# Performance work log

Hardware: AMD Instinct MI355X
Metric: run time of the kernel (lower is better)

## Reference

```python
import jax, jax.numpy as jnp
import numpy as np

B, H, C, G = 65536, 1024, 2, 2


def setup_inputs() -> dict:
    key = jax.random.key(0)
    ks = jax.random.split(key, 9)
    s = 1.0 / np.sqrt(H)
    return {
        "X": jax.random.normal(ks[0], (B, H), jnp.float32),
        "W_phi": jax.random.normal(ks[1], (H, H), jnp.float32) * s,
        "b_phi": jax.random.normal(ks[2], (H,), jnp.float32) * s,
        "W_groups": jax.random.normal(ks[3], (G, C, H), jnp.float32) * s,
        "b_groups": jax.random.normal(ks[4], (G, C), jnp.float32) * s,
        "W_joint": jax.random.normal(ks[5], (C, H), jnp.float32) * s,
        "b_joint": jax.random.normal(ks[6], (C,), jnp.float32) * s,
        "D": jax.random.randint(ks[7], (B,), 0, G, jnp.int32),
        "D_agn": jax.random.randint(ks[8], (B,), 0, G, jnp.int32),  # models random.random() < ratio
    }


def reference(X, W_phi, b_phi, W_groups, b_groups, W_joint, b_joint, D, D_agn):
    # phi feature extractor: Linear(H -> H)
    phi = X @ W_phi.T + b_phi  # [B, H]
    # Compute both experts' outputs (G=2 is tiny), then gather per-sample.
    all_preds = jnp.einsum("bh,gch->bgc", phi, W_groups) + b_groups[None]  # [B, G, C]
    group_specific = jnp.take_along_axis(all_preds, D[:, None, None].astype(jnp.int32), axis=1)[:, 0]  # [B, C]
    group_agnostic = jnp.take_along_axis(all_preds, D_agn[:, None, None].astype(jnp.int32), axis=1)[:, 0]  # [B, C]
    joint = phi @ W_joint.T + b_joint  # [B, C]
    return (joint, group_specific, group_agnostic)
```

## Files before the change

kernel.cpp:

```cpp
#include <hip/hip_runtime.h>

#define HDIM 1024
#define NR 6

__global__ __launch_bounds__(256) void precompute_kernel(
    const float* __restrict__ Wphi, const float* __restrict__ bphi,
    const float* __restrict__ Wg,  const float* __restrict__ bg,
    const float* __restrict__ Wj,  const float* __restrict__ bj,
    float* __restrict__ A, float* __restrict__ biasEff)
{
    __shared__ float red[256][NR];
    const int t = threadIdx.x;

    if (blockIdx.x == 64) {
        __shared__ float rb[256];
        for (int r = 0; r < NR; ++r) {
            const float* w2 = (r < 2) ? (Wj + r * HDIM) : (Wg + (r - 2) * HDIM);
            float s = 0.f;
            for (int h = t; h < HDIM; h += 256) s += w2[h] * bphi[h];
            rb[t] = s; __syncthreads();
            for (int off = 128; off > 0; off >>= 1) {
                if (t < off) rb[t] += rb[t + off];
                __syncthreads();
            }
            if (t == 0) {
                float b2 = (r < 2) ? bj[r] : bg[r - 2];
                biasEff[r] = rb[0] + b2;
            }
            __syncthreads();
        }
        return;
    }

    const int cb  = blockIdx.x;
    const int col = cb * 16 + (t & 15);
    const int ks  = t >> 4;

    float acc[NR];
    #pragma unroll
    for (int r = 0; r < NR; ++r) acc[r] = 0.f;

    const int h0 = ks * 64;
    #pragma unroll 4
    for (int i = 0; i < 64; ++i) {
        const int h = h0 + i;
        const float w = Wphi[(size_t)h * HDIM + col];
        acc[0] += Wj[h]            * w;
        acc[1] += Wj[HDIM + h]     * w;
        acc[2] += Wg[h]            * w;
        acc[3] += Wg[HDIM + h]     * w;
        acc[4] += Wg[2 * HDIM + h] * w;
        acc[5] += Wg[3 * HDIM + h] * w;
    }
    #pragma unroll
    for (int r = 0; r < NR; ++r) red[t][r] = acc[r];
    __syncthreads();

    if (t < 16 * NR) {
        const int c = t & 15;
        const int r = t >> 4;
        float s = 0.f;
        #pragma unroll
        for (int k = 0; k < 16; ++k) s += red[k * 16 + c][r];
        A[r * HDIM + cb * 16 + c] = s;
    }
}

__global__ __launch_bounds__(256, 3) void main_kernel(
    const float* __restrict__ X, const int* __restrict__ D,
    const int* __restrict__ Dagn,
    const float* __restrict__ A, const float* __restrict__ biasEff,
    float* __restrict__ out, int B)
{
    const int lane  = threadIdx.x & 63;
    const int wave  = threadIdx.x >> 6;
    const int gwave = blockIdx.x * 4 + wave;
    const int nwav  = gridDim.x * 4;

    float4 a[NR][4];
    #pragma unroll
    for (int r = 0; r < NR; ++r) {
        const float4* Ar = (const float4*)(A + r * HDIM);
        #pragma unroll
        for (int j = 0; j < 4; ++j) a[r][j] = Ar[lane + 64 * j];
    }
    float be[NR];
    #pragma unroll
    for (int r = 0; r < NR; ++r) be[r] = biasEff[r];

    for (int b = gwave; b < B; b += nwav) {
        const float4* xr = (const float4*)(X + (size_t)b * HDIM);
        float4 x[4];
        #pragma unroll
        for (int j = 0; j < 4; ++j) x[j] = xr[lane + 64 * j];

        float acc[NR];
        #pragma unroll
        for (int r = 0; r < NR; ++r) {
            float s = 0.f;
            #pragma unroll
            for (int j = 0; j < 4; ++j) {
                s += x[j].x * a[r][j].x + x[j].y * a[r][j].y
                   + x[j].z * a[r][j].z + x[j].w * a[r][j].w;
            }
            acc[r] = s;
        }

        #pragma unroll
        for (int r = 0; r < NR; ++r) {
            float v = acc[r];
            #pragma unroll
            for (int off = 32; off > 0; off >>= 1)
                v += __shfl_xor(v, off, 64);
            acc[r] = v;
        }

        if (lane == 0) {
            const int d  = D[b]    & 1;
            const int da = Dagn[b] & 1;
            float y[NR];
            #pragma unroll
            for (int r = 0; r < NR; ++r) y[r] = acc[r] + be[r];
            float2* o = (float2*)out;
            o[b]         = make_float2(y[0], y[1]);
            o[B + b]     = make_float2(y[2 + 2 * d],  y[3 + 2 * d]);
            o[2 * B + b] = make_float2(y[2 + 2 * da], y[3 + 2 * da]);
        }
    }
}

extern "C" void kernel_launch(void* const* d_in, const int* in_sizes, int n_in,
                              void* d_out, int out_size, void* d_ws, size_t ws_size,
                              hipStream_t stream) {
    const float* X    = (const float*)d_in[0];
    const float* Wphi = (const float*)d_in[1];
    const float* bphi = (const float*)d_in[2];
    const float* Wg   = (const float*)d_in[3];
    const float* bg   = (const float*)d_in[4];
    const float* Wj   = (const float*)d_in[5];
    const float* bj   = (const float*)d_in[6];
    const int*   D    = (const int*)d_in[7];
    const int*   Dagn = (const int*)d_in[8];
    float* out = (float*)d_out;

    const int B = in_sizes[7];

    float* A       = (float*)d_ws;
    float* biasEff = A + NR * HDIM;

    precompute_kernel<<<65, 256, 0, stream>>>(Wphi, bphi, Wg, bg, Wj, bj, A, biasEff);
    main_kernel<<<768, 256, 0, stream>>>(X, D, Dagn, A, biasEff, out, B);
}
```

Before: 389.5 us.

## Double-buffer X row loads in main kernel and widen precompute grid

The main kernel now software-pipelines its loop: it loads the next row of X into a second register buffer while computing the current row, and it reads D/Dagn early. This is meant to hide global-memory latency on a bandwidth-bound GEMV-like pass. The precompute kernel is split across 128 blocks of 8 columns instead of 64 blocks of 16, and the bias reduction uses wave shuffles instead of a shared-memory tree. The extra register buffer raises register pressure, which could reduce occupancy under launch_bounds(256,3).

```diff
diff --git a/kernel.cpp b/kernel.cpp
--- a/kernel.cpp
+++ b/kernel.cpp
@@ -9,60 +9,65 @@
     const float* __restrict__ Wj,  const float* __restrict__ bj,
     float* __restrict__ A, float* __restrict__ biasEff)
 {
-    __shared__ float red[256][NR];
     const int t = threadIdx.x;
 
-    if (blockIdx.x == 64) {
-        __shared__ float rb[256];
-        for (int r = 0; r < NR; ++r) {
-            const float* w2 = (r < 2) ? (Wj + r * HDIM) : (Wg + (r - 2) * HDIM);
+    if (blockIdx.x == 128) {
+        const int lane = t & 63;
+        const int w    = t >> 6;
+        for (int r = w; r < NR; r += 4) {
+            const float* w2 = (r < 2) ? (Wj + (size_t)r * HDIM)
+                                      : (Wg + (size_t)(r - 2) * HDIM);
+            const float4* w4 = (const float4*)w2;
+            const float4* p4 = (const float4*)bphi;
             float s = 0.f;
-            for (int h = t; h < HDIM; h += 256) s += w2[h] * bphi[h];
-            rb[t] = s; __syncthreads();
-            for (int off = 128; off > 0; off >>= 1) {
-                if (t < off) rb[t] += rb[t + off];
-                __syncthreads();
+            #pragma unroll
+            for (int j = 0; j < 4; ++j) {
+                const float4 av = w4[lane + 64 * j];
+                const float4 bv = p4[lane + 64 * j];
+                s += av.x * bv.x + av.y * bv.y + av.z * bv.z + av.w * bv.w;
             }
-            if (t == 0) {
-                float b2 = (r < 2) ? bj[r] : bg[r - 2];
-                biasEff[r] = rb[0] + b2;
-            }
-            __syncthreads();
+            #pragma unroll
+            for (int off = 32; off > 0; off >>= 1)
+                s += __shfl_xor(s, off, 64);
+            if (lane == 0)
+                biasEff[r] = s + ((r < 2) ? bj[r] : bg[r - 2]);
         }
         return;
     }
 
     const int cb  = blockIdx.x;
-    const int col = cb * 16 + (t & 15);
-    const int ks  = t >> 4;
+    const int col = cb * 8 + (t & 7);
+    const int ks  = t >> 3;
+    const int h0  = ks * 32;
 
     float acc[NR];
     #pragma unroll
     for (int r = 0; r < NR; ++r) acc[r] = 0.f;
 
-    const int h0 = ks * 64;
-    #pragma unroll 4
-    for (int i = 0; i < 64; ++i) {
+    #pragma unroll 8
+    for (int i = 0; i < 32; ++i) {
         const int h = h0 + i;
-        const float w = Wphi[(size_t)h * HDIM + col];
-        acc[0] += Wj[h]            * w;
-        acc[1] += Wj[HDIM + h]     * w;
-        acc[2] += Wg[h]            * w;
-        acc[3] += Wg[HDIM + h]     * w;
-        acc[4] += Wg[2 * HDIM + h] * w;
-        acc[5] += Wg[3 * HDIM + h] * w;
+        const float wv = Wphi[(size_t)h * HDIM + col];
+        acc[0] += Wj[h]            * wv;
+        acc[1] += Wj[HDIM + h]     * wv;
+        acc[2] += Wg[h]            * wv;
+        acc[3] += Wg[HDIM + h]     * wv;
+        acc[4] += Wg[2 * HDIM + h] * wv;
+        acc[5] += Wg[3 * HDIM + h] * wv;
     }
+
+    __shared__ float red[256][NR];
     #pragma unroll
     for (int r = 0; r < NR; ++r) red[t][r] = acc[r];
     __syncthreads();
 
-    if (t < 16 * NR) {
-        const int c = t & 15;
-        const int r = t >> 4;
+    if (t < 8 * NR) {
+        const int c = t & 7;
+        const int r = t >> 3;
         float s = 0.f;
         #pragma unroll
-        for (int k = 0; k < 16; ++k) s += red[k * 16 + c][r];
-        A[r * HDIM + cb * 16 + c] = s;
+        for (int k = 0; k < 32; ++k) s += red[k * 8 + c][r];
+        A[(size_t)r * HDIM + cb * 8 + c] = s;
     }
 }
 
@@ -80,7 +85,7 @@
     float4 a[NR][4];
     #pragma unroll
     for (int r = 0; r < NR; ++r) {
-        const float4* Ar = (const float4*)(A + r * HDIM);
+        const float4* Ar = (const float4*)(A + (size_t)r * HDIM);
         #pragma unroll
         for (int j = 0; j < 4; ++j) a[r][j] = Ar[lane + 64 * j];
     }
@@ -88,45 +93,69 @@
     #pragma unroll
     for (int r = 0; r < NR; ++r) be[r] = biasEff[r];
 
-    for (int b = gwave; b < B; b += nwav) {
-        const float4* xr = (const float4*)(X + (size_t)b * HDIM);
-        float4 x[4];
+    if (gwave >= B) return;
+
+    float4 x0[4], x1[4];
+    {
+        const float4* xr = (const float4*)(X + (size_t)gwave * HDIM);
         #pragma unroll
-        for (int j = 0; j < 4; ++j) x[j] = xr[lane + 64 * j];
+        for (int j = 0; j < 4; ++j) x0[j] = xr[lane + 64 * j];
+    }
 
-        float acc[NR];
-        #pragma unroll
-        for (int r = 0; r < NR; ++r) {
-            float s = 0.f;
+#define PROCESS(bb, xx)                                                     \
+    {                                                                       \
+        const int d_  = D[bb] & 1;      \
+        const int da_ = Dagn[bb] & 1;    \
+        float acc[NR];                                                      \
+        _Pragma("unroll")                                                   \
+        for (int r = 0; r < NR; ++r) {                                      \
+            float s = 0.f;                                                  \
+            _Pragma("unroll")                                               \
+            for (int j = 0; j < 4; ++j)                                     \
+                s += xx[j].x * a[r][j].x + xx[j].y * a[r][j].y              \
+                   + xx[j].z * a[r][j].z + xx[j].w * a[r][j].w;             \
+            acc[r] = s;                                                     \
+        }                                                                   \
+        _Pragma("unroll")                                                   \
+        for (int r = 0; r < NR; ++r) {                                      \
+            float v = acc[r];                                               \
+            _Pragma("unroll")                                               \
+            for (int off = 32; off > 0; off >>= 1)                          \
+                v += __shfl_xor(v, off, 64);                                \
+            acc[r] = v;                                                     \
+        }                                                                   \
+        if (lane == 0) {                                                    \
+            float2* o = (float2*)out;                                       \
+            o[bb]         = make_float2(acc[0] + be[0], acc[1] + be[1]);    \
+            o[B + bb]     = make_float2(acc[2 + 2 * d_]  + be[2 + 2 * d_],  \
+                                        acc[3 + 2 * d_]  + be[3 + 2 * d_]); \
+            o[2 * B + bb] = make_float2(acc[2 + 2 * da_] + be[2 + 2 * da_], \
+                                        acc[3 + 2 * da_] + be[3 + 2 * da_]);\
+        }                                                                   \
+    }
+
+    int b = gwave;
+    while (true) {
+        const int b1 = b + nwav;
+        if (b1 < B) {
+            const float4* xr = (const float4*)(X + (size_t)b1 * HDIM);
             #pragma unroll
-            for (int j = 0; j < 4; ++j) {
-                s += x[j].x * a[r][j].x + x[j].y * a[r][j].y
-                   + x[j].z * a[r][j].z + x[j].w * a[r][j].w;
-            }
-            acc[r] = s;
+            for (int j = 0; j < 4; ++j) x1[j] = xr[lane + 64 * j];
         }
+        PROCESS(b, x0)
+        if (b1 >= B) break;
 
-        #pragma unroll
-        for (int r = 0; r < NR; ++r) {
-            float v = acc[r];
+        const int b2 = b1 + nwav;
+        if (b2 < B) {
+            const float4* xr = (const float4*)(X + (size_t)b2 * HDIM);
             #pragma unroll
-            for (int off = 32; off > 0; off >>= 1)
-                v += __shfl_xor(v, off, 64);
-            acc[r] = v;
+            for (int j = 0; j < 4; ++j) x0[j] = xr[lane + 64 * j];
         }
-
-        if (lane == 0) {
-            const int d  = D[b]    & 1;
-            const int da = Dagn[b] & 1;
-            float y[NR];
-            #pragma unroll
-            for (int r = 0; r < NR; ++r) y[r] = acc[r] + be[r];
-            float2* o = (float2*)out;
-            o[b]         = make_float2(y[0], y[1]);
-            o[B + b]     = make_float2(y[2 + 2 * d],  y[3 + 2 * d]);
-            o[2 * B + b] = make_float2(y[2 + 2 * da], y[3 + 2 * da]);
-        }
+        PROCESS(b1, x1)
+        if (b2 >= B) break;
+        b = b2;
     }
+#undef PROCESS
 }
 
 extern "C" void kernel_launch(void* const* d_in, const int* in_sizes, int n_in,
@@ -148,6 +177,6 @@
     float* A       = (float*)d_ws;
     float* biasEff = A + NR * HDIM;
 
-    precompute_kernel<<<65, 256, 0, stream>>>(Wphi, bphi, Wg, bg, Wj, bj, A, biasEff);
+    precompute_kernel<<<129, 256, 0, stream>>>(Wphi, bphi, Wg, bg, Wj, bj, A, biasEff);
     main_kernel<<<768, 256, 0, stream>>>(X, D, Dagn, A, biasEff, out, B);
 }
```

Measured after the change: 380.8 us. 1.02x faster.
